# Kernel optimization log

Hardware: AMD Instinct MI355X
Metric: run time of the kernel (lower is better)

The kernel has to match this reference:

```python
import jax, jax.numpy as jnp
import numpy as np


def setup_inputs() -> dict:
    B, N, D, M = 512, 128, 768, 32  # bags, num_class, embed_dim, max bag size
    rng = np.random.default_rng(0)
    sizes = rng.integers(8, 25, size=B)  # variable bag sizes in [8, 24], all <= M
    offsets = np.concatenate([[0], np.cumsum(sizes)]).astype(np.int32)
    nsum = int(offsets[-1])
    scope = np.stack([offsets[:-1], offsets[1:]], axis=1)  # (B, 2) [start, end)

    key = jax.random.key(0)
    k1, k2, k3 = jax.random.split(key, 3)
    rep = jax.random.normal(k1, (nsum, D), dtype=jnp.float32)
    fc_weight = jax.random.normal(k2, (N, D), dtype=jnp.float32) * 0.02
    fc_bias = jax.random.normal(k3, (N,), dtype=jnp.float32) * 0.02
    return {
        "rep": rep,
        "fc_weight": fc_weight,
        "fc_bias": fc_bias,
        "scope": jnp.asarray(scope),
        "max_bag": M,
    }


def reference(rep, fc_weight, fc_bias, scope, max_bag):
    """IntraBagAttention forward (train=False, bag_size=0 branch), ragged bags
    rewritten as padded/masked dense ops.

    rep:       (nsum, D) sentence-encoder outputs
    fc_weight: (N, D), fc_bias: (N,)
    scope:     (B, 2) int [start, end) per bag; max_bag: static int pad bound
    returns:   (B, N) per-relation bag scores
    """
    nsum = rep.shape[0]
    starts = scope[:, 0]
    sizes = scope[:, 1] - scope[:, 0]
    pos = jnp.arange(max_bag)
    idx = jnp.clip(starts[:, None] + pos[None, :], 0, nsum - 1)  # (B, M)
    valid = pos[None, :] < sizes[:, None]                        # (B, M)
    bag = rep[idx]                                               # (B, M, D)

    # att_score = rep @ fc.weight.data.T ; .data => no grad through this use
    w_att = jax.lax.stop_gradient(fc_weight)
    att = jnp.einsum('bmd,nd->bnm', bag, w_att)                  # (B, N, M)
    att = jnp.where(valid[:, None, :], att, -jnp.inf)
    sm = jax.nn.softmax(att, axis=-1)                            # per-bag softmax over sentences

    # weighted segment sum: one attended rep per relation per bag
    rfer = jnp.einsum('bnm,bmd->bnd', sm, bag)                   # (B, N, D)

    # fc(rep_for_each_rel) -> (B, N, N); softmax over classes; take diagonal
    full = jnp.einsum('bnd,kd->bnk', rfer, fc_weight) + fc_bias  # (B, N, N)
    probs = jax.nn.softmax(full, axis=-1)
    return jnp.diagonal(probs, axis1=1, axis2=2)                 # (B, N)
```

## Files before the change

### kernel.cpp

```cpp
#include <hip/hip_runtime.h>
#include <math.h>

#define B_BAGS 512
#define N_REL  128
#define D_DIM  768

typedef __attribute__((ext_vector_type(8))) short  bf16x8;
typedef __attribute__((ext_vector_type(4))) float  f32x4;

__device__ inline unsigned pack_hi(float f0, float f1) {
    return __builtin_amdgcn_perm(__float_as_uint(f1), __float_as_uint(f0), 0x07060302u);
}
__device__ inline float trunc_res(float f) {
    return f - __uint_as_float(__float_as_uint(f) & 0xFFFF0000u);
}

__global__ void build_bfrag(const float* __restrict__ W, unsigned* __restrict__ Bfrag) {
    int flat = blockIdx.x * 256 + threadIdx.x;
    int lane = flat & 63;
    int tile = (flat >> 6) & 7;
    int s    = flat >> 9;
    int n  = tile * 16 + (lane & 15);
    int k0 = s * 32 + (lane >> 4) * 8;
    const float* src = &W[n * D_DIM + k0];
    float f[8];
    #pragma unroll
    for (int j = 0; j < 8; ++j) f[j] = src[j];
    unsigned hi[4], lo[4];
    #pragma unroll
    for (int q = 0; q < 4; ++q) {
        hi[q] = pack_hi(f[2*q], f[2*q+1]);
        lo[q] = pack_hi(trunc_res(f[2*q]), trunc_res(f[2*q+1]));
    }
    unsigned base = (unsigned)(((s * 8 + tile) * 2) * 64 + lane) * 4;
    *(uint4*)&Bfrag[base]          = make_uint4(hi[0], hi[1], hi[2], hi[3]);
    *(uint4*)&Bfrag[base + 64 * 4] = make_uint4(lo[0], lo[1], lo[2], lo[3]);
}

__global__ __launch_bounds__(256, 8) void h_gemm(
    const float*    __restrict__ rep,
    const unsigned* __restrict__ Bfrag,
    float*          __restrict__ Hp,
    int nsum, int hstride)
{
    __shared__ unsigned As[2][16][68];

    const int t     = threadIdx.x;
    const int strip = blockIdx.x;
    const int chunk = blockIdx.y;

    const int wv   = t >> 6;
    const int lane = t & 63;
    const int nl15 = lane & 15;
    const int lg   = lane >> 4;

    const int srow = t >> 4;
    const int scq  = t & 15;
    int grow = strip * 16 + srow;
    grow = (grow > nsum - 1) ? (nsum - 1) : grow;
    const float* srp = &rep[(size_t)grow * D_DIM + chunk * 384 + scq * 8];

    f32x4 acc[2][2];
    #pragma unroll
    for (int ntl = 0; ntl < 2; ++ntl) {
        acc[ntl][0] = f32x4{0.f, 0.f, 0.f, 0.f};
        acc[ntl][1] = f32x4{0.f, 0.f, 0.f, 0.f};
    }

    #pragma unroll
    for (int st = 0; st < 3; ++st) {
        if (st) __syncthreads();
        {
            const float4 v0 = *(const float4*)&srp[st * 128];
            const float4 v1 = *(const float4*)&srp[st * 128 + 4];
            const float f[8] = {v0.x, v0.y, v0.z, v0.w, v1.x, v1.y, v1.z, v1.w};
            unsigned hi[4], lo[4];
            #pragma unroll
            for (int w = 0; w < 4; ++w) {
                hi[w] = pack_hi(f[2*w], f[2*w+1]);
                lo[w] = pack_hi(trunc_res(f[2*w]), trunc_res(f[2*w+1]));
            }
            *(uint4*)&As[0][srow][scq * 4] = make_uint4(hi[0], hi[1], hi[2], hi[3]);
            *(uint4*)&As[1][srow][scq * 4] = make_uint4(lo[0], lo[1], lo[2], lo[3]);
        }
        __syncthreads();

        #pragma unroll
        for (int g = 0; g < 4; ++g) {
            const int gs = chunk * 12 + st * 4 + g;
            const bf16x8 ah = *(const bf16x8*)&As[0][nl15][g * 16 + lg * 4];
            const bf16x8 al = *(const bf16x8*)&As[1][nl15][g * 16 + lg * 4];
            #pragma unroll
            for (int ntl = 0; ntl < 2; ++ntl) {
                const int nt = wv * 2 + ntl;
                const bf16x8 bh = *(const bf16x8*)&Bfrag[((gs * 8 + nt) * 2 + 0) * 256 + lane * 4];
                const bf16x8 bl = *(const bf16x8*)&Bfrag[((gs * 8 + nt) * 2 + 1) * 256 + lane * 4];
                acc[ntl][0] = __builtin_amdgcn_mfma_f32_16x16x32_bf16(ah, bh, acc[ntl][0], 0, 0, 0);
                acc[ntl][1] = __builtin_amdgcn_mfma_f32_16x16x32_bf16(ah, bl, acc[ntl][1], 0, 0, 0);
                acc[ntl][1] = __builtin_amdgcn_mfma_f32_16x16x32_bf16(al, bh, acc[ntl][1], 0, 0, 0);
            }
        }
    }

    float* H = Hp + (size_t)chunk * hstride;
    const int rowb = strip * 16 + lg * 4;
    #pragma unroll
    for (int ntl = 0; ntl < 2; ++ntl) {
        const int col = (wv * 2 + ntl) * 16 + nl15;
        #pragma unroll
        for (int r = 0; r < 4; ++r)
            H[(size_t)(rowb + r) * N_REL + col] = acc[ntl][0][r] + acc[ntl][1][r];
    }
}

__global__ __launch_bounds__(512, 2) void bag_out(
    const float* __restrict__ Hp, int hstride,
    const float* __restrict__ bias,
    const int*   __restrict__ scope,
    float*       __restrict__ out,
    int nsum)
{
    __shared__ unsigned Gfrag[8 * 2 * 64 * 4];
    __shared__ unsigned SMfrag[8 * 2 * 64 * 4];

    const int t = threadIdx.x;
    const int b = blockIdx.x;
    const int start = scope[2 * b];
    const int size  = scope[2 * b + 1] - start;

    const int wv   = t >> 6;
    const int lane = t & 63;
    const int nl15 = lane & 15;
    const int lg   = lane >> 4;
    const int T    = wv;

    float gv[2][4], smv[2][4];
    #pragma unroll
    for (int mt = 0; mt < 2; ++mt)
        #pragma unroll
        for (int r = 0; r < 4; ++r) {
            int row = start + mt * 16 + lg * 4 + r;
            row = (row > nsum - 1) ? (nsum - 1) : row;
            const float* p = &Hp[(size_t)row * N_REL + T * 16 + nl15];
            gv[mt][r] = p[0] + p[(size_t)hstride];
        }

    float vmax = -INFINITY;
    #pragma unroll
    for (int mt = 0; mt < 2; ++mt)
        #pragma unroll
        for (int r = 0; r < 4; ++r) {
            const int m = mt * 16 + lg * 4 + r;
            if (m < size) vmax = fmaxf(vmax, gv[mt][r]);
        }
    vmax = fmaxf(vmax, __shfl_xor(vmax, 16));
    vmax = fmaxf(vmax, __shfl_xor(vmax, 32));

    float ssum = 0.f;
    #pragma unroll
    for (int mt = 0; mt < 2; ++mt)
        #pragma unroll
        for (int r = 0; r < 4; ++r) {
            const int m = mt * 16 + lg * 4 + r;
            float e = (m < size) ? __expf(gv[mt][r] - vmax) : 0.f;
            smv[mt][r] = e;
            ssum += e;
        }
    ssum += __shfl_xor(ssum, 16);
    ssum += __shfl_xor(ssum, 32);
    const float inv = 1.f / ssum;
    #pragma unroll
    for (int mt = 0; mt < 2; ++mt)
        #pragma unroll
        for (int r = 0; r < 4; ++r) smv[mt][r] *= inv;

    #pragma unroll
    for (int mt = 0; mt < 2; ++mt)
        #pragma unroll
        for (int rp = 0; rp < 4; rp += 2) {
            const int m     = mt * 16 + lg * 4 + rp;
            const int lane2 = (m >> 3) * 16 + nl15;
            const int word  = (m >> 1) & 3;
            const int ihi = ((T * 2 + 0) * 64 + lane2) * 4 + word;
            const int ilo = ((T * 2 + 1) * 64 + lane2) * 4 + word;
            Gfrag[ihi]  = pack_hi(gv[mt][rp], gv[mt][rp + 1]);
            Gfrag[ilo]  = pack_hi(trunc_res(gv[mt][rp]), trunc_res(gv[mt][rp + 1]));
            SMfrag[ihi] = pack_hi(smv[mt][rp], smv[mt][rp + 1]);
            SMfrag[ilo] = pack_hi(trunc_res(smv[mt][rp]), trunc_res(smv[mt][rp + 1]));
        }
    __syncthreads();

    float bias_r[8];
    #pragma unroll
    for (int ct = 0; ct < 8; ++ct) bias_r[ct] = bias[ct * 16 + nl15];

    f32x4 facc[8];
    #pragma unroll
    for (int ct = 0; ct < 8; ++ct) facc[ct] = f32x4{0.f, 0.f, 0.f, 0.f};

    const bf16x8 ah2 = *(const bf16x8*)&SMfrag[((T * 2 + 0) * 64 + lane) * 4];
    const bf16x8 al2 = *(const bf16x8*)&SMfrag[((T * 2 + 1) * 64 + lane) * 4];
    #pragma unroll
    for (int ct = 0; ct < 8; ++ct) {
        const bf16x8 bh = *(const bf16x8*)&Gfrag[((ct * 2 + 0) * 64 + lane) * 4];
        const bf16x8 bl = *(const bf16x8*)&Gfrag[((ct * 2 + 1) * 64 + lane) * 4];
        facc[ct] = __builtin_amdgcn_mfma_f32_16x16x32_bf16(ah2, bh, facc[ct], 0, 0, 0);
        facc[ct] = __builtin_amdgcn_mfma_f32_16x16x32_bf16(ah2, bl, facc[ct], 0, 0, 0);
        facc[ct] = __builtin_amdgcn_mfma_f32_16x16x32_bf16(al2, bh, facc[ct], 0, 0, 0);
    }

    #pragma unroll
    for (int r = 0; r < 4; ++r) {
        float s[8];
        #pragma unroll
        for (int ct = 0; ct < 8; ++ct) s[ct] = facc[ct][r] + bias_r[ct];

        float mx = s[0];
        #pragma unroll
        for (int ct = 1; ct < 8; ++ct) mx = fmaxf(mx, s[ct]);
        mx = fmaxf(mx, __shfl_xor(mx, 1));
        mx = fmaxf(mx, __shfl_xor(mx, 2));
        mx = fmaxf(mx, __shfl_xor(mx, 4));
        mx = fmaxf(mx, __shfl_xor(mx, 8));

        float l = 0.f;
        #pragma unroll
        for (int ct = 0; ct < 8; ++ct) l += __expf(s[ct] - mx);
        l += __shfl_xor(l, 1);
        l += __shfl_xor(l, 2);
        l += __shfl_xor(l, 4);
        l += __shfl_xor(l, 8);

        const int nl = lg * 4 + r;
        float sd = s[0];
        #pragma unroll
        for (int ct = 1; ct < 8; ++ct) sd = (ct == T) ? s[ct] : sd;
        if (nl15 == nl) {
            out[b * N_REL + T * 16 + nl] = __expf(sd - mx) / l;
        }
    }
}

extern "C" void kernel_launch(void* const* d_in, const int* in_sizes, int n_in,
                              void* d_out, int out_size, void* d_ws, size_t ws_size,
                              hipStream_t stream) {
    const float* rep   = (const float*)d_in[0];
    const float* W     = (const float*)d_in[1];
    const float* bias  = (const float*)d_in[2];
    const int*   scope = (const int*)d_in[3];

    const int nsum    = in_sizes[0] / D_DIM;
    const int strips  = (nsum + 15) >> 4;
    const int hstride = strips * 16 * N_REL;

    unsigned* Bfrag = (unsigned*)d_ws;
    float*    Hp    = (float*)((char*)d_ws + 393216);

    build_bfrag<<<48, 256, 0, stream>>>(W, Bfrag);
    h_gemm<<<dim3(strips, 2), 256, 0, stream>>>(rep, Bfrag, Hp, nsum, hstride);
    bag_out<<<B_BAGS, 512, 0, stream>>>(Hp, hstride, bias, scope,
                                        (float*)d_out, nsum);
}
```

Measured before the change: 93.25 us.

## Double GEMM row tile to 32 and split K into four chunks

Result: slower. 95.39 us (+2.3%).

```diff
diff --git a/kernel.cpp b/kernel.cpp
--- a/kernel.cpp
+++ b/kernel.cpp
@@ -4,6 +4,7 @@
 #define B_BAGS 512
 #define N_REL  128
 #define D_DIM  768
+#define NCHUNK 4
 
 typedef __attribute__((ext_vector_type(8))) short  bf16x8;
 typedef __attribute__((ext_vector_type(4))) float  f32x4;
@@ -37,13 +38,13 @@
     *(uint4*)&Bfrag[base + 64 * 4] = make_uint4(lo[0], lo[1], lo[2], lo[3]);
 }
 
-__global__ __launch_bounds__(256, 8) void h_gemm(
+__global__ __launch_bounds__(256, 4) void h_gemm(
     const float*    __restrict__ rep,
     const unsigned* __restrict__ Bfrag,
     float*          __restrict__ Hp,
     int nsum, int hstride)
 {
-    __shared__ unsigned As[2][16][68];
+    __shared__ unsigned As[2][32][36];
 
     const int t     = threadIdx.x;
     const int strip = blockIdx.x;
@@ -54,25 +55,27 @@
     const int nl15 = lane & 15;
     const int lg   = lane >> 4;
 
-    const int srow = t >> 4;
-    const int scq  = t & 15;
-    int grow = strip * 16 + srow;
+    const int srow = t >> 3;
+    const int scq  = t & 7;
+    int grow = strip * 32 + srow;
     grow = (grow > nsum - 1) ? (nsum - 1) : grow;
-    const float* srp = &rep[(size_t)grow * D_DIM + chunk * 384 + scq * 8];
-
-    f32x4 acc[2][2];
-    #pragma unroll
-    for (int ntl = 0; ntl < 2; ++ntl) {
-        acc[ntl][0] = f32x4{0.f, 0.f, 0.f, 0.f};
-        acc[ntl][1] = f32x4{0.f, 0.f, 0.f, 0.f};
-    }
+    const float* srp = &rep[(size_t)grow * D_DIM + chunk * 192 + scq * 8];
+
+    f32x4 acc[2][2][2];
+    #pragma unroll
+    for (int mt = 0; mt < 2; ++mt)
+        #pragma unroll
+        for (int ntl = 0; ntl < 2; ++ntl) {
+            acc[mt][ntl][0] = f32x4{0.f, 0.f, 0.f, 0.f};
+            acc[mt][ntl][1] = f32x4{0.f, 0.f, 0.f, 0.f};
+        }
 
     #pragma unroll
     for (int st = 0; st < 3; ++st) {
         if (st) __syncthreads();
         {
-            const float4 v0 = *(const float4*)&srp[st * 128];
-            const float4 v1 = *(const float4*)&srp[st * 128 + 4];
+            const float4 v0 = *(const float4*)&srp[st * 64];
+            const float4 v1 = *(const float4*)&srp[st * 64 + 4];
             const float f[8] = {v0.x, v0.y, v0.z, v0.w, v1.x, v1.y, v1.z, v1.w};
             unsigned hi[4], lo[4];
             #pragma unroll
@@ -86,30 +89,41 @@
         __syncthreads();
 
         #pragma unroll
-        for (int g = 0; g < 4; ++g) {
-            const int gs = chunk * 12 + st * 4 + g;
-            const bf16x8 ah = *(const bf16x8*)&As[0][nl15][g * 16 + lg * 4];
-            const bf16x8 al = *(const bf16x8*)&As[1][nl15][g * 16 + lg * 4];
+        for (int g = 0; g < 2; ++g) {
+            const int gs = chunk * 6 + st * 2 + g;
+            bf16x8 ah[2], al[2];
+            #pragma unroll
+            for (int mt = 0; mt < 2; ++mt) {
+                const int arow = mt * 16 + nl15;
+                ah[mt] = *(const bf16x8*)&As[0][arow][g * 16 + lg * 4];
+                al[mt] = *(const bf16x8*)&As[1][arow][g * 16 + lg * 4];
+            }
             #pragma unroll
             for (int ntl = 0; ntl < 2; ++ntl) {
                 const int nt = wv * 2 + ntl;
                 const bf16x8 bh = *(const bf16x8*)&Bfrag[((gs * 8 + nt) * 2 + 0) * 256 + lane * 4];
                 const bf16x8 bl = *(const bf16x8*)&Bfrag[((gs * 8 + nt) * 2 + 1) * 256 + lane * 4];
-                acc[ntl][0] = __builtin_amdgcn_mfma_f32_16x16x32_bf16(ah, bh, acc[ntl][0], 0, 0, 0);
-                acc[ntl][1] = __builtin_amdgcn_mfma_f32_16x16x32_bf16(ah, bl, acc[ntl][1], 0, 0, 0);
-                acc[ntl][1] = __builtin_amdgcn_mfma_f32_16x16x32_bf16(al, bh, acc[ntl][1], 0, 0, 0);
+                #pragma unroll
+                for (int mt = 0; mt < 2; ++mt) {
+                    acc[mt][ntl][0] = __builtin_amdgcn_mfma_f32_16x16x32_bf16(ah[mt], bh, acc[mt][ntl][0], 0, 0, 0);
+                    acc[mt][ntl][1] = __builtin_amdgcn_mfma_f32_16x16x32_bf16(ah[mt], bl, acc[mt][ntl][1], 0, 0, 0);
+                    acc[mt][ntl][1] = __builtin_amdgcn_mfma_f32_16x16x32_bf16(al[mt], bh, acc[mt][ntl][1], 0, 0, 0);
+                }
             }
         }
     }
 
     float* H = Hp + (size_t)chunk * hstride;
-    const int rowb = strip * 16 + lg * 4;
-    #pragma unroll
-    for (int ntl = 0; ntl < 2; ++ntl) {
-        const int col = (wv * 2 + ntl) * 16 + nl15;
-        #pragma unroll
-        for (int r = 0; r < 4; ++r)
-            H[(size_t)(rowb + r) * N_REL + col] = acc[ntl][0][r] + acc[ntl][1][r];
+    #pragma unroll
+    for (int mt = 0; mt < 2; ++mt) {
+        const int rowb = strip * 32 + mt * 16 + lg * 4;
+        #pragma unroll
+        for (int ntl = 0; ntl < 2; ++ntl) {
+            const int col = (wv * 2 + ntl) * 16 + nl15;
+            #pragma unroll
+            for (int r = 0; r < 4; ++r)
+                H[(size_t)(rowb + r) * N_REL + col] = acc[mt][ntl][0][r] + acc[mt][ntl][1][r];
+        }
     }
 }
 
@@ -142,7 +156,8 @@
             int row = start + mt * 16 + lg * 4 + r;
             row = (row > nsum - 1) ? (nsum - 1) : row;
             const float* p = &Hp[(size_t)row * N_REL + T * 16 + nl15];
-            gv[mt][r] = p[0] + p[(size_t)hstride];
+            gv[mt][r] = (p[0] + p[(size_t)hstride])
+                      + (p[(size_t)hstride * 2] + p[(size_t)hstride * 3]);
         }
 
     float vmax = -INFINITY;
@@ -250,14 +265,14 @@
     const int*   scope = (const int*)d_in[3];
 
     const int nsum    = in_sizes[0] / D_DIM;
-    const int strips  = (nsum + 15) >> 4;
-    const int hstride = strips * 16 * N_REL;
+    const int strips  = (nsum + 31) >> 5;
+    const int hstride = strips * 32 * N_REL;
 
     unsigned* Bfrag = (unsigned*)d_ws;
     float*    Hp    = (float*)((char*)d_ws + 393216);
 
     build_bfrag<<<48, 256, 0, stream>>>(W, Bfrag);
-    h_gemm<<<dim3(strips, 2), 256, 0, stream>>>(rep, Bfrag, Hp, nsum, hstride);
+    h_gemm<<<dim3(strips, NCHUNK), 256, 0, stream>>>(rep, Bfrag, Hp, nsum, hstride);
     bag_out<<<B_BAGS, 512, 0, stream>>>(Hp, hstride, bias, scope,
                                         (float*)d_out, nsum);
 }
```
